# Optimization experiments

Measured on AMD Instinct MI355X. Metric: run time of the kernel, lower is better.

Reference implementation:

```python
import jax, jax.numpy as jnp
import numpy as np

N_NODES = 1_000_000
N_EDGES = 26_000_000


def setup_inputs() -> dict:
    key = jax.random.key(0)
    ks = jax.random.split(key, 10)
    x = jax.random.normal(ks[0], (N_NODES, 3), dtype=jnp.float32)
    edge_index = jax.random.randint(ks[1], (2, N_EDGES), 0, N_NODES, dtype=jnp.int64)
    edge_attr = jax.random.normal(ks[2], (N_EDGES, 1), dtype=jnp.float32)
    u = jax.random.normal(ks[3], (1, 8), dtype=jnp.float32)
    batch = jnp.zeros((N_NODES,), dtype=jnp.int64)
    # node_mlp params: Lin(6,16) -> ReLU -> Lin(16,16) -> ReLU -> Lin(16,3)
    s1 = 1.0 / np.sqrt(6.0)
    s2 = 1.0 / np.sqrt(16.0)
    W1 = jax.random.uniform(ks[4], (6, 16), minval=-s1, maxval=s1, dtype=jnp.float32)
    b1 = jax.random.uniform(ks[5], (16,), minval=-s1, maxval=s1, dtype=jnp.float32)
    W2 = jax.random.uniform(ks[6], (16, 16), minval=-s2, maxval=s2, dtype=jnp.float32)
    b2 = jax.random.uniform(ks[7], (16,), minval=-s2, maxval=s2, dtype=jnp.float32)
    W3 = jax.random.uniform(ks[8], (16, 3), minval=-s2, maxval=s2, dtype=jnp.float32)
    b3 = jax.random.uniform(ks[9], (3,), minval=-s2, maxval=s2, dtype=jnp.float32)
    return {"x": x, "edge_index": edge_index, "edge_attr": edge_attr, "u": u,
            "batch": batch, "W1": W1, "b1": b1, "W2": W2, "b2": b2, "W3": W3, "b3": b3}


def reference(x, edge_index, edge_attr, u, batch, W1, b1, W2, b2, W3, b3):
    row, col = edge_index[0], edge_index[1]
    # gather source-node features along edges, scatter-sum into target nodes
    agg = jax.ops.segment_sum(x[row], col, num_segments=x.shape[0])  # [N, 3]
    h = jnp.concatenate([x, agg], axis=1)  # [N, 6]
    h = jax.nn.relu(h @ W1 + b1)
    h = jax.nn.relu(h @ W2 + b2)
    return h @ W3 + b3  # [N, 3]
```

## Files before the change

kernel.cpp:

```cpp
#include <hip/hip_runtime.h>


#define SH     12
#define TILE   4096
#define MAXNB  256
#define NBLK   512
#define THR    1024
#define SPLITK 4


__global__ __launch_bounds__(THR) void hist_kernel(
    const int* __restrict__ key, int* __restrict__ hist,
    int nb, int chunk, int n_edges)
{
    __shared__ int lh[MAXNB];
    const int t = threadIdx.x, b = blockIdx.x;
    for (int k = t; k < nb; k += THR) lh[k] = 0;
    __syncthreads();

    long long s = (long long)b * chunk;
    long long e = s + chunk; if (e > n_edges) e = n_edges;
    if (s < e) {
        const int n = (int)(e - s);
        const int n4 = n >> 2;
        const int4* __restrict__ k4p = reinterpret_cast<const int4*>(key + s);
        for (int i = t; i < n4; i += THR) {
            int4 c = k4p[i];
            atomicAdd(&lh[(unsigned)c.x >> SH], 1);
            atomicAdd(&lh[(unsigned)c.y >> SH], 1);
            atomicAdd(&lh[(unsigned)c.z >> SH], 1);
            atomicAdd(&lh[(unsigned)c.w >> SH], 1);
        }
        for (int i = (n4 << 2) + t; i < n; i += THR)
            atomicAdd(&lh[(unsigned)key[s + i] >> SH], 1);
    }
    __syncthreads();
    for (int k = t; k < nb; k += THR) hist[(size_t)b * nb + k] = lh[k];
}

__global__ __launch_bounds__(NBLK) void scan_blocks_kernel(
    int* __restrict__ hist, int* __restrict__ keyTotal, int nb)
{
    __shared__ int sd[NBLK];
    const int t = threadIdx.x, k = blockIdx.x;
    const int v = hist[(size_t)t * nb + k];
    sd[t] = v; __syncthreads();
#pragma unroll
    for (int off = 1; off < NBLK; off <<= 1) {
        int a = (t >= off) ? sd[t - off] : 0;
        __syncthreads();
        sd[t] += a;
        __syncthreads();
    }
    hist[(size_t)t * nb + k] = sd[t] - v;
    if (t == NBLK - 1) keyTotal[k] = sd[t];
}

__global__ __launch_bounds__(1024) void scan_keys_kernel(
    const int* __restrict__ keyTotal, int* __restrict__ keyStart, int nb)
{
    __shared__ int sd[1024];
    const int t = threadIdx.x;
    const int v = (t < nb) ? keyTotal[t] : 0;
    sd[t] = v; __syncthreads();
#pragma unroll
    for (int off = 1; off < 1024; off <<= 1) {
        int a = (t >= off) ? sd[t - off] : 0;
        __syncthreads();
        sd[t] += a;
        __syncthreads();
    }
    if (t < nb) keyStart[t] = sd[t] - v;
    if (t == 0) keyStart[nb] = sd[1023];
}

__global__ __launch_bounds__(THR) void scatter_kernel(
    const int* __restrict__ key, const int* __restrict__ other,
    const int* __restrict__ hist, const int* __restrict__ keyStart,
    unsigned* __restrict__ packed, int nb, int chunk, int n_edges)
{
    __shared__ int lc[MAXNB];
    const int t = threadIdx.x, b = blockIdx.x;
    for (int k = t; k < nb; k += THR)
        lc[k] = keyStart[k] + hist[(size_t)b * nb + k];
    __syncthreads();

    long long s = (long long)b * chunk;
    long long e = s + chunk; if (e > n_edges) e = n_edges;
    if (s < e) {
        const int n = (int)(e - s);
        const int n4 = n >> 2;
        const int4* __restrict__ k4p = reinterpret_cast<const int4*>(key + s);
        const int4* __restrict__ o4p = reinterpret_cast<const int4*>(other + s);
        for (int i = t; i < n4; i += THR) {
            int4 c = k4p[i];
            int4 r = o4p[i];
            int p;
            p = atomicAdd(&lc[(unsigned)c.x >> SH], 1);
            packed[p] = ((unsigned)r.x << SH) | ((unsigned)c.x & (TILE - 1));
            p = atomicAdd(&lc[(unsigned)c.y >> SH], 1);
            packed[p] = ((unsigned)r.y << SH) | ((unsigned)c.y & (TILE - 1));
            p = atomicAdd(&lc[(unsigned)c.z >> SH], 1);
            packed[p] = ((unsigned)r.z << SH) | ((unsigned)c.z & (TILE - 1));
            p = atomicAdd(&lc[(unsigned)c.w >> SH], 1);
            packed[p] = ((unsigned)r.w << SH) | ((unsigned)c.w & (TILE - 1));
        }
        for (int i = (n4 << 2) + t; i < n; i += THR) {
            int c = key[s + i], r = other[s + i];
            int p = atomicAdd(&lc[(unsigned)c >> SH], 1);
            packed[p] = ((unsigned)r << SH) | ((unsigned)c & (TILE - 1));
        }
    }
}


__global__ __launch_bounds__(256) void pad_x_kernel(
    const float* __restrict__ x, float4* __restrict__ x4, int n)
{
    const int stride = gridDim.x * 256;
    for (int i = blockIdx.x * 256 + threadIdx.x; i < n; i += stride) {
        float4 v;
        v.x = x[3 * i + 0];
        v.y = x[3 * i + 1];
        v.z = x[3 * i + 2];
        v.w = 0.0f;
        x4[i] = v;
    }
}


__global__ __launch_bounds__(THR) void agg_partial_kernel(
    const unsigned* __restrict__ packed, const float4* __restrict__ x4,
    const int* __restrict__ keyStart, float* __restrict__ partial,
    int n_nodes, int nb)
{
    __shared__ float acc[TILE * 3];
    const int t = threadIdx.x;
    const int k  = blockIdx.x % nb;
    const int sl = blockIdx.x / nb;
    for (int f = t; f < TILE * 3; f += THR) acc[f] = 0.0f;
    __syncthreads();

    const int s0 = keyStart[k], e0 = keyStart[k + 1];
    const long long len = e0 - s0;
    const int s = s0 + (int)(len * sl / SPLITK);
    const int e = s0 + (int)(len * (sl + 1) / SPLITK);

    int i = s + t;
    for (; i + 3 * THR < e; i += 4 * THR) {
        unsigned p0 = packed[i];
        unsigned p1 = packed[i + THR];
        unsigned p2 = packed[i + 2 * THR];
        unsigned p3 = packed[i + 3 * THR];
        float4 v0 = x4[p0 >> SH];
        float4 v1 = x4[p1 >> SH];
        float4 v2 = x4[p2 >> SH];
        float4 v3 = x4[p3 >> SH];
        int j0 = (int)(p0 & (TILE - 1)) * 3;
        int j1 = (int)(p1 & (TILE - 1)) * 3;
        int j2 = (int)(p2 & (TILE - 1)) * 3;
        int j3 = (int)(p3 & (TILE - 1)) * 3;
        atomicAdd(&acc[j0 + 0], v0.x); atomicAdd(&acc[j0 + 1], v0.y); atomicAdd(&acc[j0 + 2], v0.z);
        atomicAdd(&acc[j1 + 0], v1.x); atomicAdd(&acc[j1 + 1], v1.y); atomicAdd(&acc[j1 + 2], v1.z);
        atomicAdd(&acc[j2 + 0], v2.x); atomicAdd(&acc[j2 + 1], v2.y); atomicAdd(&acc[j2 + 2], v2.z);
        atomicAdd(&acc[j3 + 0], v3.x); atomicAdd(&acc[j3 + 1], v3.y); atomicAdd(&acc[j3 + 2], v3.z);
    }
    for (; i < e; i += THR) {
        unsigned p = packed[i];
        float4 v = x4[p >> SH];
        int j = (int)(p & (TILE - 1)) * 3;
        atomicAdd(&acc[j + 0], v.x);
        atomicAdd(&acc[j + 1], v.y);
        atomicAdd(&acc[j + 2], v.z);
    }
    __syncthreads();

    const long long base = (long long)k << SH;
    long long lim = (long long)n_nodes - base;
    if (lim > TILE) lim = TILE;
    if (lim <= 0) return;
    float* __restrict__ dst = partial + ((size_t)sl * n_nodes + base) * 3;
    const int fl = (int)lim * 3;
    for (int f = t; f < fl; f += THR) dst[f] = acc[f];
}


__global__ __launch_bounds__(256) void merge_mlp_kernel(
    const float* __restrict__ partial, const float* __restrict__ x,
    const float* __restrict__ W1, const float* __restrict__ b1,
    const float* __restrict__ W2, const float* __restrict__ b2,
    const float* __restrict__ W3, const float* __restrict__ b3,
    float* __restrict__ out, int n_nodes)
{
    __shared__ float sW1[96], sb1[16], sW2[256], sb2[16], sW3[48], sb3[3];
    const int t = threadIdx.x;
    if (t < 96)  sW1[t] = W1[t];
    if (t < 16)  sb1[t] = b1[t];
    sW2[t] = W2[t];
    if (t < 16)  sb2[t] = b2[t];
    if (t < 48)  sW3[t] = W3[t];
    if (t < 3)   sb3[t] = b3[t];
    __syncthreads();

    const int i = blockIdx.x * 256 + t;
    if (i >= n_nodes) return;

    float a0 = 0.0f, a1 = 0.0f, a2 = 0.0f;
#pragma unroll
    for (int sl = 0; sl < SPLITK; ++sl) {
        const float* __restrict__ p = partial + ((size_t)sl * n_nodes + i) * 3;
        a0 += p[0]; a1 += p[1]; a2 += p[2];
    }

    float in6[6];
    in6[0] = x[3 * i + 0];
    in6[1] = x[3 * i + 1];
    in6[2] = x[3 * i + 2];
    in6[3] = a0;
    in6[4] = a1;
    in6[5] = a2;

    float h1[16];
#pragma unroll
    for (int j = 0; j < 16; ++j) {
        float s = sb1[j];
#pragma unroll
        for (int k = 0; k < 6; ++k) s = fmaf(in6[k], sW1[k * 16 + j], s);
        h1[j] = fmaxf(s, 0.0f);
    }
    float h2[16];
#pragma unroll
    for (int j = 0; j < 16; ++j) {
        float s = sb2[j];
#pragma unroll
        for (int k = 0; k < 16; ++k) s = fmaf(h1[k], sW2[k * 16 + j], s);
        h2[j] = fmaxf(s, 0.0f);
    }
    float o0 = sb3[0], o1 = sb3[1], o2 = sb3[2];
#pragma unroll
    for (int j = 0; j < 16; ++j) {
        o0 = fmaf(h2[j], sW3[j * 3 + 0], o0);
        o1 = fmaf(h2[j], sW3[j * 3 + 1], o1);
        o2 = fmaf(h2[j], sW3[j * 3 + 2], o2);
    }
    out[3 * i + 0] = o0;
    out[3 * i + 1] = o1;
    out[3 * i + 2] = o2;
}


__global__ __launch_bounds__(THR) void bucket_agg_mlp_kernel(
    const unsigned* __restrict__ packed, const float* __restrict__ x,
    const int* __restrict__ keyStart,
    const float* __restrict__ W1, const float* __restrict__ b1,
    const float* __restrict__ W2, const float* __restrict__ b2,
    const float* __restrict__ W3, const float* __restrict__ b3,
    float* __restrict__ out, int n_nodes)
{
    __shared__ float acc[TILE * 3];
    __shared__ float sW1[96], sb1[16], sW2[256], sb2[16], sW3[48], sb3[3];
    const int t = threadIdx.x, k = blockIdx.x;

    if (t < 96)  sW1[t] = W1[t];
    if (t < 16)  sb1[t] = b1[t];
    if (t < 256) sW2[t] = W2[t];
    if (t >= 256 && t < 272) sb2[t - 256] = b2[t - 256];
    if (t >= 272 && t < 320) sW3[t - 272] = W3[t - 272];
    if (t >= 320 && t < 323) sb3[t - 320] = b3[t - 320];
    for (int f = t; f < TILE * 3; f += THR) acc[f] = 0.0f;
    __syncthreads();

    const int s = keyStart[k];
    const int e = keyStart[k + 1];
    int i = s + t;
    for (; i + 3 * THR < e; i += 4 * THR) {
        unsigned p0 = packed[i];
        unsigned p1 = packed[i + THR];
        unsigned p2 = packed[i + 2 * THR];
        unsigned p3 = packed[i + 3 * THR];
        const float* xs0 = x + 3ll * (p0 >> SH);
        const float* xs1 = x + 3ll * (p1 >> SH);
        const float* xs2 = x + 3ll * (p2 >> SH);
        const float* xs3 = x + 3ll * (p3 >> SH);
        float a0 = xs0[0], b0 = xs0[1], c0 = xs0[2];
        float a1 = xs1[0], b1v = xs1[1], c1 = xs1[2];
        float a2 = xs2[0], b2v = xs2[1], c2 = xs2[2];
        float a3 = xs3[0], b3v = xs3[1], c3 = xs3[2];
        int j0 = (int)(p0 & (TILE - 1)) * 3;
        int j1 = (int)(p1 & (TILE - 1)) * 3;
        int j2 = (int)(p2 & (TILE - 1)) * 3;
        int j3 = (int)(p3 & (TILE - 1)) * 3;
        atomicAdd(&acc[j0 + 0], a0); atomicAdd(&acc[j0 + 1], b0);  atomicAdd(&acc[j0 + 2], c0);
        atomicAdd(&acc[j1 + 0], a1); atomicAdd(&acc[j1 + 1], b1v); atomicAdd(&acc[j1 + 2], c1);
        atomicAdd(&acc[j2 + 0], a2); atomicAdd(&acc[j2 + 1], b2v); atomicAdd(&acc[j2 + 2], c2);
        atomicAdd(&acc[j3 + 0], a3); atomicAdd(&acc[j3 + 1], b3v); atomicAdd(&acc[j3 + 2], c3);
    }
    for (; i < e; i += THR) {
        const unsigned p = packed[i];
        const float* __restrict__ xs = x + 3ll * (p >> SH);
        const int j = (int)(p & (TILE - 1)) * 3;
        atomicAdd(&acc[j + 0], xs[0]);
        atomicAdd(&acc[j + 1], xs[1]);
        atomicAdd(&acc[j + 2], xs[2]);
    }
    __syncthreads();

    const long long base = (long long)k << SH;
    long long lim = (long long)n_nodes - base;
    if (lim > TILE) lim = TILE;
    if (lim <= 0) return;

    for (int j = t; j < (int)lim; j += THR) {
        const long long node = base + j;
        float in6[6];
        in6[0] = x[3 * node + 0];
        in6[1] = x[3 * node + 1];
        in6[2] = x[3 * node + 2];
        in6[3] = acc[3 * j + 0];
        in6[4] = acc[3 * j + 1];
        in6[5] = acc[3 * j + 2];

        float h1[16];
#pragma unroll
        for (int q = 0; q < 16; ++q) {
            float sv = sb1[q];
#pragma unroll
            for (int r = 0; r < 6; ++r) sv = fmaf(in6[r], sW1[r * 16 + q], sv);
            h1[q] = fmaxf(sv, 0.0f);
        }
        float h2[16];
#pragma unroll
        for (int q = 0; q < 16; ++q) {
            float sv = sb2[q];
#pragma unroll
            for (int r = 0; r < 16; ++r) sv = fmaf(h1[r], sW2[r * 16 + q], sv);
            h2[q] = fmaxf(sv, 0.0f);
        }
        float o0 = sb3[0], o1 = sb3[1], o2 = sb3[2];
#pragma unroll
        for (int q = 0; q < 16; ++q) {
            o0 = fmaf(h2[q], sW3[q * 3 + 0], o0);
            o1 = fmaf(h2[q], sW3[q * 3 + 1], o1);
            o2 = fmaf(h2[q], sW3[q * 3 + 2], o2);
        }
        out[3 * node + 0] = o0;
        out[3 * node + 1] = o1;
        out[3 * node + 2] = o2;
    }
}


__global__ __launch_bounds__(256) void edge_scatter_kernel(
    const int* __restrict__ rows, const int* __restrict__ cols,
    const float* __restrict__ x, float* __restrict__ agg, int n_edges)
{
    const long long tid = (long long)blockIdx.x * blockDim.x + threadIdx.x;
    const long long stride = (long long)gridDim.x * blockDim.x;
    for (long long i = tid; i < n_edges; i += stride) {
        int r = rows[i], c = cols[i];
        const float* xs = x + 3ll * r; float* a = agg + 3ll * c;
        atomicAdd(a + 0, xs[0]); atomicAdd(a + 1, xs[1]); atomicAdd(a + 2, xs[2]);
    }
}

__global__ __launch_bounds__(256) void node_mlp_kernel(
    const float* __restrict__ x,
    const float* __restrict__ W1, const float* __restrict__ b1,
    const float* __restrict__ W2, const float* __restrict__ b2,
    const float* __restrict__ W3, const float* __restrict__ b3,
    float* __restrict__ out, int n_nodes)
{
    __shared__ float sW1[96], sb1[16], sW2[256], sb2[16], sW3[48], sb3[3];
    const int t = threadIdx.x;
    if (t < 96)  sW1[t] = W1[t];
    if (t < 16)  sb1[t] = b1[t];
    sW2[t] = W2[t];
    if (t < 16)  sb2[t] = b2[t];
    if (t < 48)  sW3[t] = W3[t];
    if (t < 3)   sb3[t] = b3[t];
    __syncthreads();

    const int i = blockIdx.x * 256 + t;
    if (i >= n_nodes) return;

    float in6[6];
    in6[0] = x[3 * i + 0];
    in6[1] = x[3 * i + 1];
    in6[2] = x[3 * i + 2];
    in6[3] = out[3 * i + 0];
    in6[4] = out[3 * i + 1];
    in6[5] = out[3 * i + 2];

    float h1[16];
#pragma unroll
    for (int j = 0; j < 16; ++j) {
        float s = sb1[j];
#pragma unroll
        for (int k = 0; k < 6; ++k) s = fmaf(in6[k], sW1[k * 16 + j], s);
        h1[j] = fmaxf(s, 0.0f);
    }
    float h2[16];
#pragma unroll
    for (int j = 0; j < 16; ++j) {
        float s = sb2[j];
#pragma unroll
        for (int k = 0; k < 16; ++k) s = fmaf(h1[k], sW2[k * 16 + j], s);
        h2[j] = fmaxf(s, 0.0f);
    }
    float o[3];
#pragma unroll
    for (int c = 0; c < 3; ++c) {
        float s = sb3[c];
#pragma unroll
        for (int j = 0; j < 16; ++j) s = fmaf(h2[j], sW3[j * 3 + c], s);
        o[c] = s;
    }
    out[3 * i + 0] = o[0];
    out[3 * i + 1] = o[1];
    out[3 * i + 2] = o[2];
}

extern "C" void kernel_launch(void* const* d_in, const int* in_sizes, int n_in,
                              void* d_out, int out_size, void* d_ws, size_t ws_size,
                              hipStream_t stream) {
    const float* x   = (const float*)d_in[0];
    const int*   ei  = (const int*)d_in[1];
    const float* W1  = (const float*)d_in[5];
    const float* b1  = (const float*)d_in[6];
    const float* W2  = (const float*)d_in[7];
    const float* b2  = (const float*)d_in[8];
    const float* W3  = (const float*)d_in[9];
    const float* b3  = (const float*)d_in[10];

    const int n_nodes = in_sizes[0] / 3;
    const int n_edges = in_sizes[1] / 2;
    const int* rows = ei;
    const int* cols = ei + n_edges;
    float* out = (float*)d_out;

    const int nb = (n_nodes + TILE - 1) >> SH;

    int chunk = (n_edges + NBLK - 1) / NBLK;
    chunk = (chunk + 3) & ~3;

    const size_t off_x4      = 0;
    const size_t off_packed  = off_x4 + (size_t)n_nodes * 16;
    const size_t off_partial = off_packed + (size_t)n_edges * 4;
    const size_t off_hist    = off_partial + (size_t)SPLITK * n_nodes * 12;
    const size_t off_kt      = off_hist + (size_t)NBLK * nb * 4;
    const size_t off_ks      = off_kt + (size_t)nb * 4;
    const size_t needA       = off_ks + (size_t)(nb + 1) * 4;

    const size_t needB = (size_t)n_edges * 4 + (size_t)NBLK * nb * 4
                       + (size_t)nb * 4 + (size_t)(nb + 1) * 4;
    const bool okA = (ws_size >= needA) && (nb <= MAXNB) && (n_nodes <= (1 << 20));
    const bool okB = (ws_size >= needB) && (nb <= MAXNB) && (n_nodes <= (1 << 20));

    if (okA) {
        float4*   x4       = (float4*)((char*)d_ws + off_x4);
        unsigned* packed   = (unsigned*)((char*)d_ws + off_packed);
        float*    partial  = (float*)((char*)d_ws + off_partial);
        int*      hist     = (int*)((char*)d_ws + off_hist);
        int*      keyTotal = (int*)((char*)d_ws + off_kt);
        int*      keyStart = (int*)((char*)d_ws + off_ks);

        pad_x_kernel<<<2048, 256, 0, stream>>>(x, x4, n_nodes);
        hist_kernel<<<NBLK, THR, 0, stream>>>(cols, hist, nb, chunk, n_edges);
        scan_blocks_kernel<<<nb, NBLK, 0, stream>>>(hist, keyTotal, nb);
        scan_keys_kernel<<<1, 1024, 0, stream>>>(keyTotal, keyStart, nb);
        scatter_kernel<<<NBLK, THR, 0, stream>>>(cols, rows, hist, keyStart,
                                                 packed, nb, chunk, n_edges);
        agg_partial_kernel<<<nb * SPLITK, THR, 0, stream>>>(
            packed, x4, keyStart, partial, n_nodes, nb);
        merge_mlp_kernel<<<(n_nodes + 255) / 256, 256, 0, stream>>>(
            partial, x, W1, b1, W2, b2, W3, b3, out, n_nodes);
    } else if (okB) {
        unsigned* packed = (unsigned*)d_ws;
        int* hist        = (int*)(packed + n_edges);
        int* keyTotal    = hist + (size_t)NBLK * nb;
        int* keyStart    = keyTotal + nb;

        hist_kernel<<<NBLK, THR, 0, stream>>>(cols, hist, nb, chunk, n_edges);
        scan_blocks_kernel<<<nb, NBLK, 0, stream>>>(hist, keyTotal, nb);
        scan_keys_kernel<<<1, 1024, 0, stream>>>(keyTotal, keyStart, nb);
        scatter_kernel<<<NBLK, THR, 0, stream>>>(cols, rows, hist, keyStart,
                                                 packed, nb, chunk, n_edges);
        bucket_agg_mlp_kernel<<<nb, THR, 0, stream>>>(
            packed, x, keyStart, W1, b1, W2, b2, W3, b3, out, n_nodes);
    } else {
        hipMemsetAsync(d_out, 0, (size_t)out_size * sizeof(float), stream);
        edge_scatter_kernel<<<8192, 256, 0, stream>>>(rows, cols, x, out, n_edges);
        node_mlp_kernel<<<(n_nodes + 255) / 256, 256, 0, stream>>>(
            x, W1, b1, W2, b2, W3, b3, out, n_nodes);
    }
}
```

Baseline: 668.5 us.

## Sort edges within each bucket by source high bits before fused aggregation

Adds a per-bucket counting-sort pass that reorders packed edges by their top 8 bits (source node high bits), so gathers of x4 within a block touch nearby source rows and get better cache locality. The split-K partial aggregation and separate merge+MLP kernel are replaced by a single fused aggregate+MLP kernel per bucket (templated for float4 or raw x). This removes the partial buffer write/read traffic but cuts parallelism from nb*4 blocks to nb blocks (about 245), and adds an extra read/write pass over all edges.

```diff
diff --git a/kernel.cpp b/kernel.cpp
--- a/kernel.cpp
+++ b/kernel.cpp
@@ -1,12 +1,11 @@
 #include <hip/hip_runtime.h>
 
 
-#define SH     12
-#define TILE   4096
-#define MAXNB  256
-#define NBLK   512
-#define THR    1024
-#define SPLITK 4
+#define SH    12
+#define TILE  4096
+#define MAXNB 256
+#define NBLK  512
+#define THR   1024
 
 
 __global__ __launch_bounds__(THR) void hist_kernel(
@@ -129,137 +128,56 @@
 }
 
 
-__global__ __launch_bounds__(THR) void agg_partial_kernel(
-    const unsigned* __restrict__ packed, const float4* __restrict__ x4,
-    const int* __restrict__ keyStart, float* __restrict__ partial,
-    int n_nodes, int nb)
-{
-    __shared__ float acc[TILE * 3];
-    const int t = threadIdx.x;
-    const int k  = blockIdx.x % nb;
-    const int sl = blockIdx.x / nb;
-    for (int f = t; f < TILE * 3; f += THR) acc[f] = 0.0f;
-    __syncthreads();
-
-    const int s0 = keyStart[k], e0 = keyStart[k + 1];
-    const long long len = e0 - s0;
-    const int s = s0 + (int)(len * sl / SPLITK);
-    const int e = s0 + (int)(len * (sl + 1) / SPLITK);
-
-    int i = s + t;
-    for (; i + 3 * THR < e; i += 4 * THR) {
-        unsigned p0 = packed[i];
-        unsigned p1 = packed[i + THR];
-        unsigned p2 = packed[i + 2 * THR];
-        unsigned p3 = packed[i + 3 * THR];
-        float4 v0 = x4[p0 >> SH];
-        float4 v1 = x4[p1 >> SH];
-        float4 v2 = x4[p2 >> SH];
-        float4 v3 = x4[p3 >> SH];
-        int j0 = (int)(p0 & (TILE - 1)) * 3;
-        int j1 = (int)(p1 & (TILE - 1)) * 3;
-        int j2 = (int)(p2 & (TILE - 1)) * 3;
-        int j3 = (int)(p3 & (TILE - 1)) * 3;
-        atomicAdd(&acc[j0 + 0], v0.x); atomicAdd(&acc[j0 + 1], v0.y); atomicAdd(&acc[j0 + 2], v0.z);
-        atomicAdd(&acc[j1 + 0], v1.x); atomicAdd(&acc[j1 + 1], v1.y); atomicAdd(&acc[j1 + 2], v1.z);
-        atomicAdd(&acc[j2 + 0], v2.x); atomicAdd(&acc[j2 + 1], v2.y); atomicAdd(&acc[j2 + 2], v2.z);
-        atomicAdd(&acc[j3 + 0], v3.x); atomicAdd(&acc[j3 + 1], v3.y); atomicAdd(&acc[j3 + 2], v3.z);
-    }
-    for (; i < e; i += THR) {
+__global__ __launch_bounds__(THR) void reorder_kernel(
+    const unsigned* __restrict__ packed, unsigned* __restrict__ packed2,
+    const int* __restrict__ keyStart)
+{
+    __shared__ int h[256];
+    __shared__ int sd[256];
+    __shared__ int cur[256];
+    const int t = threadIdx.x, cb = blockIdx.x;
+    if (t < 256) h[t] = 0;
+    __syncthreads();
+
+    const int s = keyStart[cb], e = keyStart[cb + 1];
+
+    for (int i = s + t; i < e; i += THR)
+        atomicAdd(&h[packed[i] >> 24], 1);
+    __syncthreads();
+
+    if (t < 256) sd[t] = h[t];
+    __syncthreads();
+#pragma unroll
+    for (int off = 1; off < 256; off <<= 1) {
+        int a = 0;
+        if (t < 256 && t >= off) a = sd[t - off];
+        __syncthreads();
+        if (t < 256) sd[t] += a;
+        __syncthreads();
+    }
+    if (t < 256) cur[t] = s + sd[t] - h[t];
+    __syncthreads();
+
+    for (int i = s + t; i < e; i += THR) {
         unsigned p = packed[i];
-        float4 v = x4[p >> SH];
-        int j = (int)(p & (TILE - 1)) * 3;
-        atomicAdd(&acc[j + 0], v.x);
-        atomicAdd(&acc[j + 1], v.y);
-        atomicAdd(&acc[j + 2], v.z);
-    }
-    __syncthreads();
-
-    const long long base = (long long)k << SH;
-    long long lim = (long long)n_nodes - base;
-    if (lim > TILE) lim = TILE;
-    if (lim <= 0) return;
-    float* __restrict__ dst = partial + ((size_t)sl * n_nodes + base) * 3;
-    const int fl = (int)lim * 3;
-    for (int f = t; f < fl; f += THR) dst[f] = acc[f];
-}
-
-
-__global__ __launch_bounds__(256) void merge_mlp_kernel(
-    const float* __restrict__ partial, const float* __restrict__ x,
+        int q = atomicAdd(&cur[p >> 24], 1);
+        packed2[q] = p;
+    }
+}
+
+
+template <bool USE_X4>
+__global__ __launch_bounds__(THR) void agg_mlp_kernel(
+    const unsigned* __restrict__ pk, const float4* __restrict__ x4,
+    const float* __restrict__ x, const int* __restrict__ keyStart,
     const float* __restrict__ W1, const float* __restrict__ b1,
     const float* __restrict__ W2, const float* __restrict__ b2,
     const float* __restrict__ W3, const float* __restrict__ b3,
     float* __restrict__ out, int n_nodes)
 {
-    __shared__ float sW1[96], sb1[16], sW2[256], sb2[16], sW3[48], sb3[3];
-    const int t = threadIdx.x;
-    if (t < 96)  sW1[t] = W1[t];
-    if (t < 16)  sb1[t] = b1[t];
-    sW2[t] = W2[t];
-    if (t < 16)  sb2[t] = b2[t];
-    if (t < 48)  sW3[t] = W3[t];
-    if (t < 3)   sb3[t] = b3[t];
-    __syncthreads();
-
-    const int i = blockIdx.x * 256 + t;
-    if (i >= n_nodes) return;
-
-    float a0 = 0.0f, a1 = 0.0f, a2 = 0.0f;
-#pragma unroll
-    for (int sl = 0; sl < SPLITK; ++sl) {
-        const float* __restrict__ p = partial + ((size_t)sl * n_nodes + i) * 3;
-        a0 += p[0]; a1 += p[1]; a2 += p[2];
-    }
-
-    float in6[6];
-    in6[0] = x[3 * i + 0];
-    in6[1] = x[3 * i + 1];
-    in6[2] = x[3 * i + 2];
-    in6[3] = a0;
-    in6[4] = a1;
-    in6[5] = a2;
-
-    float h1[16];
-#pragma unroll
-    for (int j = 0; j < 16; ++j) {
-        float s = sb1[j];
-#pragma unroll
-        for (int k = 0; k < 6; ++k) s = fmaf(in6[k], sW1[k * 16 + j], s);
-        h1[j] = fmaxf(s, 0.0f);
-    }
-    float h2[16];
-#pragma unroll
-    for (int j = 0; j < 16; ++j) {
-        float s = sb2[j];
-#pragma unroll
-        for (int k = 0; k < 16; ++k) s = fmaf(h1[k], sW2[k * 16 + j], s);
-        h2[j] = fmaxf(s, 0.0f);
-    }
-    float o0 = sb3[0], o1 = sb3[1], o2 = sb3[2];
-#pragma unroll
-    for (int j = 0; j < 16; ++j) {
-        o0 = fmaf(h2[j], sW3[j * 3 + 0], o0);
-        o1 = fmaf(h2[j], sW3[j * 3 + 1], o1);
-        o2 = fmaf(h2[j], sW3[j * 3 + 2], o2);
-    }
-    out[3 * i + 0] = o0;
-    out[3 * i + 1] = o1;
-    out[3 * i + 2] = o2;
-}
-
-
-__global__ __launch_bounds__(THR) void bucket_agg_mlp_kernel(
-    const unsigned* __restrict__ packed, const float* __restrict__ x,
-    const int* __restrict__ keyStart,
-    const float* __restrict__ W1, const float* __restrict__ b1,
-    const float* __restrict__ W2, const float* __restrict__ b2,
-    const float* __restrict__ W3, const float* __restrict__ b3,
-    float* __restrict__ out, int n_nodes)
-{
     __shared__ float acc[TILE * 3];
     __shared__ float sW1[96], sb1[16], sW2[256], sb2[16], sW3[48], sb3[3];
-    const int t = threadIdx.x, k = blockIdx.x;
+    const int t = threadIdx.x, cb = blockIdx.x;
 
     if (t < 96)  sW1[t] = W1[t];
     if (t < 16)  sb1[t] = b1[t];
@@ -270,42 +188,35 @@
     for (int f = t; f < TILE * 3; f += THR) acc[f] = 0.0f;
     __syncthreads();
 
-    const int s = keyStart[k];
-    const int e = keyStart[k + 1];
+    const int s = keyStart[cb], e = keyStart[cb + 1];
+
+    auto add1 = [&](unsigned p) {
+        const int j = (int)(p & (TILE - 1)) * 3;
+        if (USE_X4) {
+            float4 v = x4[p >> SH];
+            atomicAdd(&acc[j + 0], v.x);
+            atomicAdd(&acc[j + 1], v.y);
+            atomicAdd(&acc[j + 2], v.z);
+        } else {
+            const float* __restrict__ xs = x + 3ll * (p >> SH);
+            atomicAdd(&acc[j + 0], xs[0]);
+            atomicAdd(&acc[j + 1], xs[1]);
+            atomicAdd(&acc[j + 2], xs[2]);
+        }
+    };
+
     int i = s + t;
     for (; i + 3 * THR < e; i += 4 * THR) {
-        unsigned p0 = packed[i];
-        unsigned p1 = packed[i + THR];
-        unsigned p2 = packed[i + 2 * THR];
-        unsigned p3 = packed[i + 3 * THR];
-        const float* xs0 = x + 3ll * (p0 >> SH);
-        const float* xs1 = x + 3ll * (p1 >> SH);
-        const float* xs2 = x + 3ll * (p2 >> SH);
-        const float* xs3 = x + 3ll * (p3 >> SH);
-        float a0 = xs0[0], b0 = xs0[1], c0 = xs0[2];
-        float a1 = xs1[0], b1v = xs1[1], c1 = xs1[2];
-        float a2 = xs2[0], b2v = xs2[1], c2 = xs2[2];
-        float a3 = xs3[0], b3v = xs3[1], c3 = xs3[2];
-        int j0 = (int)(p0 & (TILE - 1)) * 3;
-        int j1 = (int)(p1 & (TILE - 1)) * 3;
-        int j2 = (int)(p2 & (TILE - 1)) * 3;
-        int j3 = (int)(p3 & (TILE - 1)) * 3;
-        atomicAdd(&acc[j0 + 0], a0); atomicAdd(&acc[j0 + 1], b0);  atomicAdd(&acc[j0 + 2], c0);
-        atomicAdd(&acc[j1 + 0], a1); atomicAdd(&acc[j1 + 1], b1v); atomicAdd(&acc[j1 + 2], c1);
-        atomicAdd(&acc[j2 + 0], a2); atomicAdd(&acc[j2 + 1], b2v); atomicAdd(&acc[j2 + 2], c2);
-        atomicAdd(&acc[j3 + 0], a3); atomicAdd(&acc[j3 + 1], b3v); atomicAdd(&acc[j3 + 2], c3);
-    }
-    for (; i < e; i += THR) {
-        const unsigned p = packed[i];
-        const float* __restrict__ xs = x + 3ll * (p >> SH);
-        const int j = (int)(p & (TILE - 1)) * 3;
-        atomicAdd(&acc[j + 0], xs[0]);
-        atomicAdd(&acc[j + 1], xs[1]);
-        atomicAdd(&acc[j + 2], xs[2]);
-    }
-    __syncthreads();
-
-    const long long base = (long long)k << SH;
+        unsigned p0 = pk[i];
+        unsigned p1 = pk[i + THR];
+        unsigned p2 = pk[i + 2 * THR];
+        unsigned p3 = pk[i + 3 * THR];
+        add1(p0); add1(p1); add1(p2); add1(p3);
+    }
+    for (; i < e; i += THR) add1(pk[i]);
+    __syncthreads();
+
+    const long long base = (long long)cb << SH;
     long long lim = (long long)n_nodes - base;
     if (lim > TILE) lim = TILE;
     if (lim <= 0) return;
@@ -443,13 +354,13 @@
     int chunk = (n_edges + NBLK - 1) / NBLK;
     chunk = (chunk + 3) & ~3;
 
-    const size_t off_x4      = 0;
-    const size_t off_packed  = off_x4 + (size_t)n_nodes * 16;
-    const size_t off_partial = off_packed + (size_t)n_edges * 4;
-    const size_t off_hist    = off_partial + (size_t)SPLITK * n_nodes * 12;
-    const size_t off_kt      = off_hist + (size_t)NBLK * nb * 4;
-    const size_t off_ks      = off_kt + (size_t)nb * 4;
-    const size_t needA       = off_ks + (size_t)(nb + 1) * 4;
+    const size_t off_x4     = 0;
+    const size_t off_packed = off_x4 + (size_t)n_nodes * 16;
+    const size_t off_pk2    = off_packed + (size_t)n_edges * 4;
+    const size_t off_hist   = off_pk2 + (size_t)n_edges * 4;
+    const size_t off_kt     = off_hist + (size_t)NBLK * nb * 4;
+    const size_t off_ks     = off_kt + (size_t)nb * 4;
+    const size_t needA      = off_ks + (size_t)(nb + 1) * 4;
 
     const size_t needB = (size_t)n_edges * 4 + (size_t)NBLK * nb * 4
                        + (size_t)nb * 4 + (size_t)(nb + 1) * 4;
@@ -459,7 +370,7 @@
     if (okA) {
         float4*   x4       = (float4*)((char*)d_ws + off_x4);
         unsigned* packed   = (unsigned*)((char*)d_ws + off_packed);
-        float*    partial  = (float*)((char*)d_ws + off_partial);
+        unsigned* packed2  = (unsigned*)((char*)d_ws + off_pk2);
         int*      hist     = (int*)((char*)d_ws + off_hist);
         int*      keyTotal = (int*)((char*)d_ws + off_kt);
         int*      keyStart = (int*)((char*)d_ws + off_ks);
@@ -470,10 +381,10 @@
         scan_keys_kernel<<<1, 1024, 0, stream>>>(keyTotal, keyStart, nb);
         scatter_kernel<<<NBLK, THR, 0, stream>>>(cols, rows, hist, keyStart,
                                                  packed, nb, chunk, n_edges);
-        agg_partial_kernel<<<nb * SPLITK, THR, 0, stream>>>(
-            packed, x4, keyStart, partial, n_nodes, nb);
-        merge_mlp_kernel<<<(n_nodes + 255) / 256, 256, 0, stream>>>(
-            partial, x, W1, b1, W2, b2, W3, b3, out, n_nodes);
+        reorder_kernel<<<nb, THR, 0, stream>>>(packed, packed2, keyStart);
+        agg_mlp_kernel<true><<<nb, THR, 0, stream>>>(packed2, x4, x, keyStart,
+                                                     W1, b1, W2, b2, W3, b3,
+                                                     out, n_nodes);
     } else if (okB) {
         unsigned* packed = (unsigned*)d_ws;
         int* hist        = (int*)(packed + n_edges);
@@ -485,8 +396,9 @@
         scan_keys_kernel<<<1, 1024, 0, stream>>>(keyTotal, keyStart, nb);
         scatter_kernel<<<NBLK, THR, 0, stream>>>(cols, rows, hist, keyStart,
                                                  packed, nb, chunk, n_edges);
-        bucket_agg_mlp_kernel<<<nb, THR, 0, stream>>>(
-            packed, x, keyStart, W1, b1, W2, b2, W3, b3, out, n_nodes);
+        agg_mlp_kernel<false><<<nb, THR, 0, stream>>>(packed, nullptr, x, keyStart,
+                                                      W1, b1, W2, b2, W3, b3,
+                                                      out, n_nodes);
     } else {
         hipMemsetAsync(d_out, 0, (size_t)out_size * sizeof(float), stream);
         edge_scatter_kernel<<<8192, 256, 0, stream>>>(rows, cols, x, out, n_edges);
```

Result: slower. 1.027 ms (+53.6%).

## Sub-bucket edges by source window to localize gathers in aggregation

Applied to the files above, without the earlier changes.

Adds a per-bucket reorder pass that sorts packed edges by the top 8 bits (source node window), then splits aggregation into 8 source windows per destination tile instead of 4 arbitrary slices. Each aggregation block gathers x4 rows from a narrow source range, which is meant to improve L2 locality of the random gathers. In exchange it adds an extra full pass reading and writing the 26M packed edges, more workspace, and twice as many partial buffers to merge. The fallback bucket path also loses its unrolled loop.

```diff
diff --git a/kernel.cpp b/kernel.cpp
--- a/kernel.cpp
+++ b/kernel.cpp
@@ -1,12 +1,12 @@
 #include <hip/hip_runtime.h>
 
 
-#define SH     12
-#define TILE   4096
-#define MAXNB  256
-#define NBLK   512
-#define THR    1024
-#define SPLITK 4
+#define SH    12
+#define TILE  4096
+#define MAXNB 256
+#define NBLK  512
+#define THR   1024
+#define NWIN  8
 
 
 __global__ __launch_bounds__(THR) void hist_kernel(
@@ -129,29 +129,69 @@
 }
 
 
-__global__ __launch_bounds__(THR) void agg_partial_kernel(
-    const unsigned* __restrict__ packed, const float4* __restrict__ x4,
-    const int* __restrict__ keyStart, float* __restrict__ partial,
+__global__ __launch_bounds__(THR) void reorder_kernel(
+    const unsigned* __restrict__ packed, unsigned* __restrict__ packed2,
+    const int* __restrict__ keyStart, int* __restrict__ subStart)
+{
+    __shared__ int h[256];
+    __shared__ int sd[256];
+    __shared__ int cur[256];
+    const int t = threadIdx.x, cb = blockIdx.x;
+    if (t < 256) h[t] = 0;
+    __syncthreads();
+
+    const int s = keyStart[cb], e = keyStart[cb + 1];
+
+    for (int i = s + t; i < e; i += THR)
+        atomicAdd(&h[packed[i] >> 24], 1);
+    __syncthreads();
+
+    if (t < 256) sd[t] = h[t];
+    __syncthreads();
+#pragma unroll
+    for (int off = 1; off < 256; off <<= 1) {
+        int a = 0;
+        if (t < 256 && t >= off) a = sd[t - off];
+        __syncthreads();
+        if (t < 256) sd[t] += a;
+        __syncthreads();
+    }
+    if (t < 256) cur[t] = s + sd[t] - h[t];
+    __syncthreads();
+
+    if (t < NWIN) subStart[cb * (NWIN + 1) + t] = cur[t * 32];
+    if (t == 0)   subStart[cb * (NWIN + 1) + NWIN] = e;
+    __syncthreads();
+
+    for (int i = s + t; i < e; i += THR) {
+        unsigned p = packed[i];
+        int q = atomicAdd(&cur[p >> 24], 1);
+        packed2[q] = p;
+    }
+}
+
+
+__global__ __launch_bounds__(THR) void agg_win_kernel(
+    const unsigned* __restrict__ packed2, const float4* __restrict__ x4,
+    const int* __restrict__ subStart, float* __restrict__ partial,
     int n_nodes, int nb)
 {
     __shared__ float acc[TILE * 3];
     const int t = threadIdx.x;
-    const int k  = blockIdx.x % nb;
-    const int sl = blockIdx.x / nb;
+    const int cb = blockIdx.x % nb;
+    const int w  = blockIdx.x / nb;
     for (int f = t; f < TILE * 3; f += THR) acc[f] = 0.0f;
     __syncthreads();
 
-    const int s0 = keyStart[k], e0 = keyStart[k + 1];
-    const long long len = e0 - s0;
-    const int s = s0 + (int)(len * sl / SPLITK);
-    const int e = s0 + (int)(len * (sl + 1) / SPLITK);
+    const int s = subStart[cb * (NWIN + 1) + w];
+    const int e = subStart[cb * (NWIN + 1) + w + 1];
 
     int i = s + t;
     for (; i + 3 * THR < e; i += 4 * THR) {
-        unsigned p0 = packed[i];
-        unsigned p1 = packed[i + THR];
-        unsigned p2 = packed[i + 2 * THR];
-        unsigned p3 = packed[i + 3 * THR];
+        unsigned p0 = packed2[i];
+        unsigned p1 = packed2[i + THR];
+        unsigned p2 = packed2[i + 2 * THR];
+        unsigned p3 = packed2[i + 3 * THR];
         float4 v0 = x4[p0 >> SH];
         float4 v1 = x4[p1 >> SH];
         float4 v2 = x4[p2 >> SH];
@@ -166,7 +206,7 @@
         atomicAdd(&acc[j3 + 0], v3.x); atomicAdd(&acc[j3 + 1], v3.y); atomicAdd(&acc[j3 + 2], v3.z);
     }
     for (; i < e; i += THR) {
-        unsigned p = packed[i];
+        unsigned p = packed2[i];
         float4 v = x4[p >> SH];
         int j = (int)(p & (TILE - 1)) * 3;
         atomicAdd(&acc[j + 0], v.x);
@@ -175,11 +215,11 @@
     }
     __syncthreads();
 
-    const long long base = (long long)k << SH;
+    const long long base = (long long)cb << SH;
     long long lim = (long long)n_nodes - base;
     if (lim > TILE) lim = TILE;
     if (lim <= 0) return;
-    float* __restrict__ dst = partial + ((size_t)sl * n_nodes + base) * 3;
+    float* __restrict__ dst = partial + ((size_t)w * n_nodes + base) * 3;
     const int fl = (int)lim * 3;
     for (int f = t; f < fl; f += THR) dst[f] = acc[f];
 }
@@ -207,8 +247,8 @@
 
     float a0 = 0.0f, a1 = 0.0f, a2 = 0.0f;
 #pragma unroll
-    for (int sl = 0; sl < SPLITK; ++sl) {
-        const float* __restrict__ p = partial + ((size_t)sl * n_nodes + i) * 3;
+    for (int w = 0; w < NWIN; ++w) {
+        const float* __restrict__ p = partial + ((size_t)w * n_nodes + i) * 3;
         a0 += p[0]; a1 += p[1]; a2 += p[2];
     }
 
@@ -272,30 +312,7 @@
 
     const int s = keyStart[k];
     const int e = keyStart[k + 1];
-    int i = s + t;
-    for (; i + 3 * THR < e; i += 4 * THR) {
-        unsigned p0 = packed[i];
-        unsigned p1 = packed[i + THR];
-        unsigned p2 = packed[i + 2 * THR];
-        unsigned p3 = packed[i + 3 * THR];
-        const float* xs0 = x + 3ll * (p0 >> SH);
-        const float* xs1 = x + 3ll * (p1 >> SH);
-        const float* xs2 = x + 3ll * (p2 >> SH);
-        const float* xs3 = x + 3ll * (p3 >> SH);
-        float a0 = xs0[0], b0 = xs0[1], c0 = xs0[2];
-        float a1 = xs1[0], b1v = xs1[1], c1 = xs1[2];
-        float a2 = xs2[0], b2v = xs2[1], c2 = xs2[2];
-        float a3 = xs3[0], b3v = xs3[1], c3 = xs3[2];
-        int j0 = (int)(p0 & (TILE - 1)) * 3;
-        int j1 = (int)(p1 & (TILE - 1)) * 3;
-        int j2 = (int)(p2 & (TILE - 1)) * 3;
-        int j3 = (int)(p3 & (TILE - 1)) * 3;
-        atomicAdd(&acc[j0 + 0], a0); atomicAdd(&acc[j0 + 1], b0);  atomicAdd(&acc[j0 + 2], c0);
-        atomicAdd(&acc[j1 + 0], a1); atomicAdd(&acc[j1 + 1], b1v); atomicAdd(&acc[j1 + 2], c1);
-        atomicAdd(&acc[j2 + 0], a2); atomicAdd(&acc[j2 + 1], b2v); atomicAdd(&acc[j2 + 2], c2);
-        atomicAdd(&acc[j3 + 0], a3); atomicAdd(&acc[j3 + 1], b3v); atomicAdd(&acc[j3 + 2], c3);
-    }
-    for (; i < e; i += THR) {
+    for (int i = s + t; i < e; i += THR) {
         const unsigned p = packed[i];
         const float* __restrict__ xs = x + 3ll * (p >> SH);
         const int j = (int)(p & (TILE - 1)) * 3;
@@ -443,13 +460,15 @@
     int chunk = (n_edges + NBLK - 1) / NBLK;
     chunk = (chunk + 3) & ~3;
 
-    const size_t off_x4      = 0;
-    const size_t off_packed  = off_x4 + (size_t)n_nodes * 16;
-    const size_t off_partial = off_packed + (size_t)n_edges * 4;
-    const size_t off_hist    = off_partial + (size_t)SPLITK * n_nodes * 12;
-    const size_t off_kt      = off_hist + (size_t)NBLK * nb * 4;
-    const size_t off_ks      = off_kt + (size_t)nb * 4;
-    const size_t needA       = off_ks + (size_t)(nb + 1) * 4;
+    const size_t off_x4     = 0;
+    const size_t off_packed = off_x4 + (size_t)n_nodes * 16;
+    const size_t off_pk2    = off_packed + (size_t)n_edges * 4;
+    const size_t off_part   = off_pk2 + (size_t)n_edges * 4;
+    const size_t off_hist   = off_part + (size_t)NWIN * n_nodes * 12;
+    const size_t off_kt     = off_hist + (size_t)NBLK * nb * 4;
+    const size_t off_ks     = off_kt + (size_t)nb * 4;
+    const size_t off_ss     = off_ks + (size_t)(nb + 1) * 4;
+    const size_t needA      = off_ss + (size_t)nb * (NWIN + 1) * 4;
 
     const size_t needB = (size_t)n_edges * 4 + (size_t)NBLK * nb * 4
                        + (size_t)nb * 4 + (size_t)(nb + 1) * 4;
@@ -459,10 +478,12 @@
     if (okA) {
         float4*   x4       = (float4*)((char*)d_ws + off_x4);
         unsigned* packed   = (unsigned*)((char*)d_ws + off_packed);
-        float*    partial  = (float*)((char*)d_ws + off_partial);
+        unsigned* packed2  = (unsigned*)((char*)d_ws + off_pk2);
+        float*    partial  = (float*)((char*)d_ws + off_part);
         int*      hist     = (int*)((char*)d_ws + off_hist);
         int*      keyTotal = (int*)((char*)d_ws + off_kt);
         int*      keyStart = (int*)((char*)d_ws + off_ks);
+        int*      subStart = (int*)((char*)d_ws + off_ss);
 
         pad_x_kernel<<<2048, 256, 0, stream>>>(x, x4, n_nodes);
         hist_kernel<<<NBLK, THR, 0, stream>>>(cols, hist, nb, chunk, n_edges);
@@ -470,8 +491,9 @@
         scan_keys_kernel<<<1, 1024, 0, stream>>>(keyTotal, keyStart, nb);
         scatter_kernel<<<NBLK, THR, 0, stream>>>(cols, rows, hist, keyStart,
                                                  packed, nb, chunk, n_edges);
-        agg_partial_kernel<<<nb * SPLITK, THR, 0, stream>>>(
-            packed, x4, keyStart, partial, n_nodes, nb);
+        reorder_kernel<<<nb, THR, 0, stream>>>(packed, packed2, keyStart, subStart);
+        agg_win_kernel<<<nb * NWIN, THR, 0, stream>>>(packed2, x4, subStart,
+                                                      partial, n_nodes, nb);
         merge_mlp_kernel<<<(n_nodes + 255) / 256, 256, 0, stream>>>(
             partial, x, W1, b1, W2, b2, W3, b3, out, n_nodes);
     } else if (okB) {
```

Result: slower. 823.4 us (+23.2%).
